# Optimization experiments

Hardware: AMD Instinct MI355X
Metric: run time of the kernel (lower is better)

Reference implementation:

```python
import jax, jax.numpy as jnp
import numpy as np

N, E = 100000, 1600000
IN, H, OUT, K = 512, 128, 128, 10
BN_EPS = 1e-5


def setup_inputs() -> dict:
    key = jax.random.key(0)
    ks = jax.random.split(key, 8)
    x = jax.random.normal(ks[0], (N, IN), dtype=jnp.float32)
    edge_index = jax.random.randint(ks[1], (2, E), 0, N, dtype=jnp.int64)
    W_enc = jax.random.normal(ks[2], (H, IN), dtype=jnp.float32) / np.sqrt(IN)
    b_enc = jnp.zeros((H,), dtype=jnp.float32)
    gammas = jax.random.normal(ks[3], (K + 1,), dtype=jnp.float32) * 0.3
    bn_gamma = jnp.ones((H,), dtype=jnp.float32)
    bn_beta = jnp.zeros((H,), dtype=jnp.float32)
    W_up = jax.random.normal(ks[4], (OUT, H), dtype=jnp.float32) / np.sqrt(H)
    b_up = jnp.zeros((OUT,), dtype=jnp.float32)
    prelu_alpha = jnp.array(0.25, dtype=jnp.float32)
    return dict(x=x, W_enc=W_enc, b_enc=b_enc, gammas=gammas,
                bn_gamma=bn_gamma, bn_beta=bn_beta, W_up=W_up, b_up=b_up,
                prelu_alpha=prelu_alpha, edge_index=edge_index, high_pass=1)


def reference(x, W_enc, b_enc, gammas, bn_gamma, bn_beta, W_up, b_up,
              prelu_alpha, edge_index, high_pass):
    n = x.shape[0]
    src, dst = edge_index[0], edge_index[1]

    # encoder (dropout p=0 -> identity)
    h = x @ W_enc.T + b_enc  # [N, H]

    # GCN-style symmetric normalization with self loops
    deg = jax.ops.segment_sum(jnp.ones_like(src, dtype=h.dtype), dst,
                              num_segments=n) + 1.0  # [N]
    w = jax.lax.rsqrt(deg[src] * deg[dst])  # [E]

    def adj(v):  # v: [N, H] -> A_hat @ v  (includes 1/deg self-loop term)
        msg = jax.ops.segment_sum(w[:, None] * v[src], dst, num_segments=n)
        return msg + v / deg[:, None]

    if high_pass:
        op = lambda v: v - adj(v)   # L_hat = I - A_hat
    else:
        op = adj

    # K-order polynomial filter: sum_k gamma_k * Op^k(h)
    def step(carry, g):
        hk, acc = carry
        hk = op(hk)
        return (hk, acc + g * hk), None

    (_, acc), _ = jax.lax.scan(step, (h, gammas[0] * h), gammas[1:])

    # BatchNorm1d over nodes (training-mode batch statistics)
    mu = jnp.mean(acc, axis=0)
    var = jnp.mean(jnp.square(acc - mu), axis=0)
    z = (acc - mu) * jax.lax.rsqrt(var + BN_EPS) * bn_gamma + bn_beta

    y = z @ W_up.T + b_up
    return jnp.where(y > 0, y, prelu_alpha * y)
```

## Files before the change

### kernel.cpp

```cpp
#include <hip/hip_runtime.h>
#include <hip/hip_fp16.h>

#define H_DIM 128
#define IN_DIM 512

typedef _Float16 half4v __attribute__((ext_vector_type(4)));
typedef _Float16 half8v __attribute__((ext_vector_type(8)));
typedef float f32x4 __attribute__((ext_vector_type(4)));

static inline size_t align256(size_t x) { return (x + 255) & ~(size_t)255; }


__global__ void count_deg_kernel(const int* __restrict__ dst, int* __restrict__ cnt, int e) {
    int i = blockIdx.x * blockDim.x + threadIdx.x;
    if (i < e) atomicAdd(&cnt[dst[i]], 1);
}

__global__ void deg_fin_kernel(const int* __restrict__ cnt, float* __restrict__ deg,
                               float* __restrict__ inv_deg, int n) {
    int i = blockIdx.x * blockDim.x + threadIdx.x;
    if (i < n) {
        float d = (float)cnt[i] + 1.0f;
        deg[i] = d;
        inv_deg[i] = 1.0f / d;
    }
}

__global__ void scan_a_kernel(const int* __restrict__ cnt, int* __restrict__ partial, int n) {
    __shared__ int sm[256];
    int i = blockIdx.x * 256 + threadIdx.x;
    sm[threadIdx.x] = (i < n) ? cnt[i] : 0;
    __syncthreads();
    for (int off = 128; off > 0; off >>= 1) {
        if (threadIdx.x < off) sm[threadIdx.x] += sm[threadIdx.x + off];
        __syncthreads();
    }
    if (threadIdx.x == 0) partial[blockIdx.x] = sm[0];
}

__global__ void scan_b_kernel(int* __restrict__ partial, int nb) {
    __shared__ int sm[512];
    int t = threadIdx.x;
    int v = (t < nb) ? partial[t] : 0;
    sm[t] = v;
    __syncthreads();
    for (int off = 1; off < 512; off <<= 1) {
        int u = (t >= off) ? sm[t - off] : 0;
        __syncthreads();
        sm[t] += u;
        __syncthreads();
    }
    if (t < nb) partial[t] = sm[t] - v;
}

__global__ void scan_c_kernel(const int* __restrict__ cnt, const int* __restrict__ partial,
                              int* __restrict__ row_start, int n) {
    __shared__ int sm[256];
    int i = blockIdx.x * 256 + threadIdx.x;
    int v = (i < n) ? cnt[i] : 0;
    sm[threadIdx.x] = v;
    __syncthreads();
    for (int off = 1; off < 256; off <<= 1) {
        int u = (threadIdx.x >= off) ? sm[threadIdx.x - off] : 0;
        __syncthreads();
        sm[threadIdx.x] += u;
        __syncthreads();
    }
    if (i < n) row_start[i + 1] = partial[blockIdx.x] + sm[threadIdx.x];
    if (i == 0) row_start[0] = 0;
}

__global__ void fill_csr_kernel(const int* __restrict__ src, const int* __restrict__ dst,
                                const float* __restrict__ deg, const int* __restrict__ row_start,
                                int* __restrict__ fill, int2* __restrict__ csr2, int e) {
    int i = blockIdx.x * blockDim.x + threadIdx.x;
    if (i < e) {
        int s = src[i], d = dst[i];
        int pos = row_start[d] + atomicAdd(&fill[d], 1);
        float w = 1.0f / sqrtf(deg[s] * deg[d]);
        csr2[pos] = make_int2(s, __float_as_int(w));
    }
}

__global__ __launch_bounds__(256) void encoder_mfma_kernel(
    const float* __restrict__ x, const float* __restrict__ W,
    const float* __restrict__ bias, const float* __restrict__ gammas,
    __half* __restrict__ h, __half* __restrict__ acc, int n) {
    __shared__ _Float16 As[64][64];
    __shared__ _Float16 Bs[128][64];
    const int tid = threadIdx.x;
    const int lane = tid & 63;
    const int wid = tid >> 6;
    const int wm = wid >> 1, wn = wid & 1;
    const int row0 = blockIdx.x * 64;
    const int lr = lane & 15;
    const int lk = (lane >> 4) * 8;
    f32x4 cacc[2][4];
#pragma unroll
    for (int a = 0; a < 2; ++a)
#pragma unroll
        for (int b = 0; b < 4; ++b) cacc[a][b] = (f32x4){0.f, 0.f, 0.f, 0.f};

    float4 xr[4], wr[8];
#pragma unroll
    for (int q = 0; q < 4; ++q) {
        int slot = tid * 4 + q;
        int r = slot >> 4, kq = (slot & 15) * 4;
        xr[q] = make_float4(0.f, 0.f, 0.f, 0.f);
        if (row0 + r < n) xr[q] = *(const float4*)&x[(size_t)(row0 + r) * IN_DIM + kq];
    }
#pragma unroll
    for (int q = 0; q < 8; ++q) {
        int slot = tid * 8 + q;
        int c = slot >> 4, kq = (slot & 15) * 4;
        wr[q] = *(const float4*)&W[(size_t)c * IN_DIM + kq];
    }

    for (int k0 = 0; k0 < IN_DIM; k0 += 64) {
#pragma unroll
        for (int q = 0; q < 4; ++q) {
            int slot = tid * 4 + q;
            int r = slot >> 4, kq = (slot & 15) * 4;
            int idx = kq ^ ((r & 7) << 3);
            half4v hv = {(_Float16)xr[q].x, (_Float16)xr[q].y, (_Float16)xr[q].z, (_Float16)xr[q].w};
            *(half4v*)&As[r][idx] = hv;
        }
#pragma unroll
        for (int q = 0; q < 8; ++q) {
            int slot = tid * 8 + q;
            int c = slot >> 4, kq = (slot & 15) * 4;
            int idx = kq ^ ((c & 7) << 3);
            half4v hv = {(_Float16)wr[q].x, (_Float16)wr[q].y, (_Float16)wr[q].z, (_Float16)wr[q].w};
            *(half4v*)&Bs[c][idx] = hv;
        }
        __syncthreads();
        if (k0 + 64 < IN_DIM) {
            int kn = k0 + 64;
#pragma unroll
            for (int q = 0; q < 4; ++q) {
                int slot = tid * 4 + q;
                int r = slot >> 4, kq = (slot & 15) * 4;
                xr[q] = make_float4(0.f, 0.f, 0.f, 0.f);
                if (row0 + r < n) xr[q] = *(const float4*)&x[(size_t)(row0 + r) * IN_DIM + kn + kq];
            }
#pragma unroll
            for (int q = 0; q < 8; ++q) {
                int slot = tid * 8 + q;
                int c = slot >> 4, kq = (slot & 15) * 4;
                wr[q] = *(const float4*)&W[(size_t)c * IN_DIM + kn + kq];
            }
        }
#pragma unroll
        for (int kk = 0; kk < 64; kk += 32) {
            half8v af[2], bf[4];
#pragma unroll
            for (int fm = 0; fm < 2; ++fm) {
                int r = wm * 32 + fm * 16 + lr;
                int kx = (kk + lk) ^ ((r & 7) << 3);
                af[fm] = *(const half8v*)&As[r][kx];
            }
#pragma unroll
            for (int fn = 0; fn < 4; ++fn) {
                int c = wn * 64 + fn * 16 + lr;
                int kx = (kk + lk) ^ ((c & 7) << 3);
                bf[fn] = *(const half8v*)&Bs[c][kx];
            }
#pragma unroll
            for (int fm = 0; fm < 2; ++fm)
#pragma unroll
                for (int fn = 0; fn < 4; ++fn)
                    cacc[fm][fn] = __builtin_amdgcn_mfma_f32_16x16x32_f16(
                        af[fm], bf[fn], cacc[fm][fn], 0, 0, 0);
        }
        __syncthreads();
    }
    const float g0 = gammas[0];
    const int orow = (lane >> 4) * 4;
#pragma unroll
    for (int fm = 0; fm < 2; ++fm) {
#pragma unroll
        for (int r = 0; r < 4; ++r) {
            int row = row0 + wm * 32 + fm * 16 + orow + r;
            if (row < n) {
#pragma unroll
                for (int fn = 0; fn < 4; ++fn) {
                    int col = wn * 64 + fn * 16 + lr;
                    float v = cacc[fm][fn][r] + bias[col];
                    h[(size_t)row * H_DIM + col] = __float2half(v);
                    acc[(size_t)row * H_DIM + col] = __float2half(g0 * v);
                }
            }
        }
    }
}

__global__ __launch_bounds__(256) void prop_kernel(
    const int* __restrict__ row_start, const int2* __restrict__ csr2,
    const float* __restrict__ inv_deg,
    const __half* __restrict__ hin, __half* __restrict__ hout,
    __half* __restrict__ acc, const float* __restrict__ gammas, int k,
    const int* __restrict__ hpp, int n) {
    const int w = threadIdx.x >> 6;
    const int l = threadIdx.x & 63;
    const int g = l >> 4;
    const int sub = l & 15;
    const int i = blockIdx.x * 4 + w;
    if (i >= n) return;
    const int beg = row_start[i], end = row_start[i + 1];
    const half8v* __restrict__ hin8 = (const half8v*)hin;
    float msg[8];
#pragma unroll
    for (int j = 0; j < 8; ++j) msg[j] = 0.f;
    int e = beg;
    for (; e + 8 <= end; e += 8) {
        int2 p0 = csr2[e + g];
        int2 p1 = csr2[e + 4 + g];
        half8v v0 = hin8[(size_t)p0.x * 16 + sub];
        half8v v1 = hin8[(size_t)p1.x * 16 + sub];
        float w0 = __int_as_float(p0.y), w1 = __int_as_float(p1.y);
#pragma unroll
        for (int j = 0; j < 8; ++j) {
            msg[j] = fmaf(w0, (float)v0[j], msg[j]);
            msg[j] = fmaf(w1, (float)v1[j], msg[j]);
        }
    }
    for (; e < end; e += 4) {
        int idx = e + g;
        int cidx = idx < end ? idx : end - 1;
        int2 p = csr2[cidx];
        float wgt = idx < end ? __int_as_float(p.y) : 0.f;
        half8v v = hin8[(size_t)p.x * 16 + sub];
#pragma unroll
        for (int j = 0; j < 8; ++j) msg[j] = fmaf(wgt, (float)v[j], msg[j]);
    }
#pragma unroll
    for (int j = 0; j < 8; ++j) {
        float m = msg[j];
        m += __shfl_xor(m, 16);
        m += __shfl_xor(m, 32);
        msg[j] = m;
    }
    const float idg = inv_deg[i];
    const half8v s8 = hin8[(size_t)i * 16 + sub];
    const int hp = *hpp;
    float hnew[8];
#pragma unroll
    for (int j = 0; j < 8; ++j) {
        float sf = (float)s8[j];
        float a = fmaf(sf, idg, msg[j]);
        hnew[j] = hp ? (sf - a) : a;
    }
    half8v* hout8 = (half8v*)hout;
    half8v* acc8 = (half8v*)acc;
    if (g == 0) {
        half8v h8;
#pragma unroll
        for (int j = 0; j < 8; ++j) h8[j] = (_Float16)hnew[j];
        hout8[(size_t)i * 16 + sub] = h8;
    } else if (g == 1) {
        const float gm = gammas[k];
        half8v av = acc8[(size_t)i * 16 + sub];
        half8v r;
#pragma unroll
        for (int j = 0; j < 8; ++j) r[j] = (_Float16)fmaf(gm, hnew[j], (float)av[j]);
        acc8[(size_t)i * 16 + sub] = r;
    }
}


__global__ __launch_bounds__(128) void bn_partial_kernel(const __half* __restrict__ acc,
                                                         float* __restrict__ sums, int n, int rpb) {
    int f = threadIdx.x;
    int r0 = blockIdx.x * rpb;
    int r1 = min(r0 + rpb, n);
    float s = 0.f, sq = 0.f;
    for (int r = r0; r < r1; ++r) {
        float v = __half2float(acc[(size_t)r * H_DIM + f]);
        s += v;
        sq = fmaf(v, v, sq);
    }
    atomicAdd(&sums[f], s);
    atomicAdd(&sums[H_DIM + f], sq);
}

__global__ __launch_bounds__(128) void bn_prep_kernel(
    const float* __restrict__ sums, const float* __restrict__ bn_gamma,
    const float* __restrict__ bn_beta, const float* __restrict__ W_up,
    const float* __restrict__ b_up, __half* __restrict__ W2h, float* __restrict__ cvec, int n) {
    __shared__ float ss[128], sh[128];
    int t = threadIdx.x;
    float nf = (float)n;
    float mu = sums[t] / nf;
    float var = sums[H_DIM + t] / nf - mu * mu;
    float sc = bn_gamma[t] / sqrtf(var + 1e-5f);
    float shv = bn_beta[t] - mu * sc;
    ss[t] = sc;
    sh[t] = shv;
    __syncthreads();
    float c = b_up[t];
    for (int hh = 0; hh < H_DIM; ++hh) {
        float wv = W_up[(size_t)t * H_DIM + hh];
        W2h[(size_t)t * H_DIM + hh] = __float2half(wv * ss[hh]);
        c = fmaf(wv, sh[hh], c);
    }
    cvec[t] = c;
}

__global__ __launch_bounds__(256) void final_mfma_kernel(
    const __half* __restrict__ accp, const __half* __restrict__ W2,
    const float* __restrict__ cvec, const float* __restrict__ alpha_p,
    float* __restrict__ out, int n) {
    __shared__ _Float16 As[64][128];
    __shared__ _Float16 Bs[128][128];
    const int tid = threadIdx.x;
    const int lane = tid & 63;
    const int wid = tid >> 6;
    const int wm = wid >> 1, wn = wid & 1;
    const int row0 = blockIdx.x * 64;
    const int lr = lane & 15;
    const int lk = (lane >> 4) * 8;
    f32x4 cacc[2][4];
#pragma unroll
    for (int a = 0; a < 2; ++a)
#pragma unroll
        for (int b = 0; b < 4; ++b) cacc[a][b] = (f32x4){0.f, 0.f, 0.f, 0.f};

#pragma unroll
    for (int q = 0; q < 4; ++q) {
        int slot = tid * 4 + q;
        int r = slot >> 4;
        int kq = (slot & 15) * 8;
        half8v av = {(_Float16)0, (_Float16)0, (_Float16)0, (_Float16)0,
                     (_Float16)0, (_Float16)0, (_Float16)0, (_Float16)0};
        if (row0 + r < n) av = *(const half8v*)&accp[(size_t)(row0 + r) * H_DIM + kq];
        int idx = kq ^ ((r & 7) << 3);
        *(half8v*)&As[r][idx] = av;
    }
#pragma unroll
    for (int q = 0; q < 8; ++q) {
        int slot = tid * 8 + q;
        int c = slot >> 4;
        int kq = (slot & 15) * 8;
        half8v wv = *(const half8v*)&W2[(size_t)c * H_DIM + kq];
        int idx = kq ^ ((c & 7) << 3);
        *(half8v*)&Bs[c][idx] = wv;
    }
    __syncthreads();
#pragma unroll
    for (int kk = 0; kk < 128; kk += 32) {
        half8v af[2], bf[4];
#pragma unroll
        for (int fm = 0; fm < 2; ++fm) {
            int r = wm * 32 + fm * 16 + lr;
            int kx = (kk + lk) ^ ((r & 7) << 3);
            af[fm] = *(const half8v*)&As[r][kx];
        }
#pragma unroll
        for (int fn = 0; fn < 4; ++fn) {
            int c = wn * 64 + fn * 16 + lr;
            int kx = (kk + lk) ^ ((c & 7) << 3);
            bf[fn] = *(const half8v*)&Bs[c][kx];
        }
#pragma unroll
        for (int fm = 0; fm < 2; ++fm)
#pragma unroll
            for (int fn = 0; fn < 4; ++fn)
                cacc[fm][fn] = __builtin_amdgcn_mfma_f32_16x16x32_f16(
                    af[fm], bf[fn], cacc[fm][fn], 0, 0, 0);
    }
    const float al = *alpha_p;
    const int orow = (lane >> 4) * 4;
#pragma unroll
    for (int fm = 0; fm < 2; ++fm) {
#pragma unroll
        for (int r = 0; r < 4; ++r) {
            int row = row0 + wm * 32 + fm * 16 + orow + r;
            if (row < n) {
#pragma unroll
                for (int fn = 0; fn < 4; ++fn) {
                    int col = wn * 64 + fn * 16 + lr;
                    float v = cacc[fm][fn][r] + cvec[col];
                    out[(size_t)row * H_DIM + col] = v > 0.f ? v : al * v;
                }
            }
        }
    }
}


extern "C" void kernel_launch(void* const* d_in, const int* in_sizes, int n_in,
                              void* d_out, int out_size, void* d_ws, size_t ws_size,
                              hipStream_t stream) {
    const float* x          = (const float*)d_in[0];
    const float* W_enc      = (const float*)d_in[1];
    const float* b_enc      = (const float*)d_in[2];
    const float* gammas     = (const float*)d_in[3];
    const float* bn_gamma   = (const float*)d_in[4];
    const float* bn_beta    = (const float*)d_in[5];
    const float* W_up       = (const float*)d_in[6];
    const float* b_up       = (const float*)d_in[7];
    const float* prelu_al   = (const float*)d_in[8];
    const int*   edge_index = (const int*)d_in[9];
    const int*   high_pass  = (const int*)d_in[10];

    const int H   = in_sizes[2];
    const int INF = in_sizes[1] / H;
    const int n   = in_sizes[0] / INF;
    const int e   = in_sizes[9] / 2;
    const int K   = in_sizes[3] - 1;

    const int* src = edge_index;
    const int* dst = edge_index + e;

    char* p = (char*)d_ws;
    auto alloc = [&](size_t bytes) -> char* { char* r = p; p += align256(bytes); return r; };
    int*    cnt       = (int*)alloc((size_t)n * 4);
    int*    fill      = (int*)alloc((size_t)n * 4);
    int*    row_start = (int*)alloc(((size_t)n + 1) * 4);
    int*    partial   = (int*)alloc(4096);
    float*  deg       = (float*)alloc((size_t)n * 4);
    float*  inv_deg   = (float*)alloc((size_t)n * 4);
    int2*   csr2      = (int2*)alloc(((size_t)e + 8) * 8);
    __half* hkA       = (__half*)alloc((size_t)n * H * 2);
    __half* hkB       = (__half*)alloc((size_t)n * H * 2);
    __half* acc       = (__half*)alloc((size_t)n * H * 2);
    float*  sums      = (float*)alloc(256 * 4);
    __half* W2h       = (__half*)alloc((size_t)H * H * 2);
    float*  cvec      = (float*)alloc((size_t)H * 4);

    hipMemsetAsync(cnt, 0, (size_t)n * 4, stream);
    hipMemsetAsync(fill, 0, (size_t)n * 4, stream);
    hipMemsetAsync(sums, 0, 256 * 4, stream);

    const int gb_e = (e + 255) / 256;
    const int gb_n = (n + 255) / 256;

    count_deg_kernel<<<gb_e, 256, 0, stream>>>(dst, cnt, e);
    deg_fin_kernel<<<gb_n, 256, 0, stream>>>(cnt, deg, inv_deg, n);
    scan_a_kernel<<<gb_n, 256, 0, stream>>>(cnt, partial, n);
    scan_b_kernel<<<1, 512, 0, stream>>>(partial, gb_n);
    scan_c_kernel<<<gb_n, 256, 0, stream>>>(cnt, partial, row_start, n);
    fill_csr_kernel<<<gb_e, 256, 0, stream>>>(src, dst, deg, row_start, fill, csr2, e);

    const int gb_m = (n + 63) / 64;
    encoder_mfma_kernel<<<gb_m, 256, 0, stream>>>(x, W_enc, b_enc, gammas, hkA, acc, n);

    __half* cur = hkA;
    __half* nxt = hkB;
    for (int k = 1; k <= K; ++k) {
        prop_kernel<<<(n + 3) / 4, 256, 0, stream>>>(row_start, csr2, inv_deg,
                                                     cur, nxt, acc, gammas, k, high_pass, n);
        __half* t = cur; cur = nxt; nxt = t;
    }

    const int nb_bn = 512;
    const int rpb = (n + nb_bn - 1) / nb_bn;
    bn_partial_kernel<<<nb_bn, 128, 0, stream>>>(acc, sums, n, rpb);
    bn_prep_kernel<<<1, 128, 0, stream>>>(sums, bn_gamma, bn_beta, W_up, b_up, W2h, cvec, n);
    final_mfma_kernel<<<gb_m, 256, 0, stream>>>(acc, W2h, cvec, prelu_al, (float*)d_out, n);
}
```

Measured before the change: 1.300 ms.

## Stage encoder tiles via direct global-to-LDS loads and unroll propagation gather

The encoder GEMM stops staging x and W through registers with a software prefetch. It now uses global_load_lds to copy swizzled fp32 x tiles and a pre-converted fp16 copy of W straight into shared memory, and converts A to fp16 when reading fragments. A small kernel that converts W to half is added, and the propagation kernel gains a 16-edge unrolled gather loop to keep more loads in flight. The trade-off is the loss of the register double-buffering overlap, a doubled LDS footprint for A, and an extra kernel launch.

```diff
diff --git a/kernel.cpp b/kernel.cpp
--- a/kernel.cpp
+++ b/kernel.cpp
@@ -9,6 +9,12 @@
 typedef float f32x4 __attribute__((ext_vector_type(4)));
 
 static inline size_t align256(size_t x) { return (x + 255) & ~(size_t)255; }
+
+__device__ inline void gload_lds16(const void* g, void* l) {
+    __builtin_amdgcn_global_load_lds(
+        (const __attribute__((address_space(1))) unsigned int*)g,
+        (__attribute__((address_space(3))) unsigned int*)l, 16, 0, 0);
+}
 
 
 __global__ void count_deg_kernel(const int* __restrict__ dst, int* __restrict__ cnt, int e) {
@@ -82,88 +88,72 @@
     }
 }
 
+__global__ void w_to_half_kernel(const float* __restrict__ W, __half* __restrict__ Wh, int total4) {
+    int i = blockIdx.x * blockDim.x + threadIdx.x;
+    if (i < total4) {
+        float4 v = *(const float4*)&W[i * 4];
+        half4v h = {(_Float16)v.x, (_Float16)v.y, (_Float16)v.z, (_Float16)v.w};
+        *(half4v*)&((_Float16*)Wh)[i * 4] = h;
+    }
+}
+
 __global__ __launch_bounds__(256) void encoder_mfma_kernel(
-    const float* __restrict__ x, const float* __restrict__ W,
+    const float* __restrict__ x, const __half* __restrict__ Wh,
     const float* __restrict__ bias, const float* __restrict__ gammas,
     __half* __restrict__ h, __half* __restrict__ acc, int n) {
-    __shared__ _Float16 As[64][64];
-    __shared__ _Float16 Bs[128][64];
+    __shared__ float As[64 * 64];
+    __shared__ _Float16 Bs[128 * 64];
     const int tid = threadIdx.x;
     const int lane = tid & 63;
     const int wid = tid >> 6;
     const int wm = wid >> 1, wn = wid & 1;
     const int row0 = blockIdx.x * 64;
     const int lr = lane & 15;
-    const int lk = (lane >> 4) * 8;
+    const int lk = lane >> 4;
     f32x4 cacc[2][4];
 #pragma unroll
     for (int a = 0; a < 2; ++a)
 #pragma unroll
         for (int b = 0; b < 4; ++b) cacc[a][b] = (f32x4){0.f, 0.f, 0.f, 0.f};
 
-    float4 xr[4], wr[8];
-#pragma unroll
-    for (int q = 0; q < 4; ++q) {
-        int slot = tid * 4 + q;
-        int r = slot >> 4, kq = (slot & 15) * 4;
-        xr[q] = make_float4(0.f, 0.f, 0.f, 0.f);
-        if (row0 + r < n) xr[q] = *(const float4*)&x[(size_t)(row0 + r) * IN_DIM + kq];
-    }
-#pragma unroll
-    for (int q = 0; q < 8; ++q) {
-        int slot = tid * 8 + q;
-        int c = slot >> 4, kq = (slot & 15) * 4;
-        wr[q] = *(const float4*)&W[(size_t)c * IN_DIM + kq];
-    }
-
     for (int k0 = 0; k0 < IN_DIM; k0 += 64) {
 #pragma unroll
         for (int q = 0; q < 4; ++q) {
-            int slot = tid * 4 + q;
-            int r = slot >> 4, kq = (slot & 15) * 4;
-            int idx = kq ^ ((r & 7) << 3);
-            half4v hv = {(_Float16)xr[q].x, (_Float16)xr[q].y, (_Float16)xr[q].z, (_Float16)xr[q].w};
-            *(half4v*)&As[r][idx] = hv;
-        }
-#pragma unroll
-        for (int q = 0; q < 8; ++q) {
-            int slot = tid * 8 + q;
-            int c = slot >> 4, kq = (slot & 15) * 4;
-            int idx = kq ^ ((c & 7) << 3);
-            half4v hv = {(_Float16)wr[q].x, (_Float16)wr[q].y, (_Float16)wr[q].z, (_Float16)wr[q].w};
-            *(half4v*)&Bs[c][idx] = hv;
-        }
-        __syncthreads();
-        if (k0 + 64 < IN_DIM) {
-            int kn = k0 + 64;
-#pragma unroll
-            for (int q = 0; q < 4; ++q) {
-                int slot = tid * 4 + q;
-                int r = slot >> 4, kq = (slot & 15) * 4;
-                xr[q] = make_float4(0.f, 0.f, 0.f, 0.f);
-                if (row0 + r < n) xr[q] = *(const float4*)&x[(size_t)(row0 + r) * IN_DIM + kn + kq];
-            }
-#pragma unroll
-            for (int q = 0; q < 8; ++q) {
-                int slot = tid * 8 + q;
-                int c = slot >> 4, kq = (slot & 15) * 4;
-                wr[q] = *(const float4*)&W[(size_t)c * IN_DIM + kn + kq];
-            }
-        }
+            int s = wid * 256 + q * 64 + lane;
+            int r = s >> 4, grp = s & 15;
+            int srow = (row0 + r < n) ? (row0 + r) : 0;
+            int col = k0 + ((grp ^ (r & 7)) << 2);
+            gload_lds16(&x[(size_t)srow * IN_DIM + col], &As[s * 4]);
+        }
+#pragma unroll
+        for (int q = 0; q < 4; ++q) {
+            int s = wid * 256 + q * 64 + lane;
+            int c = s >> 3, grp = s & 7;
+            int col = k0 + ((grp ^ (c & 7)) << 3);
+            gload_lds16(&((const _Float16*)Wh)[(size_t)c * IN_DIM + col], &Bs[s * 8]);
+        }
+        __syncthreads();
 #pragma unroll
         for (int kk = 0; kk < 64; kk += 32) {
             half8v af[2], bf[4];
 #pragma unroll
             for (int fm = 0; fm < 2; ++fm) {
                 int r = wm * 32 + fm * 16 + lr;
-                int kx = (kk + lk) ^ ((r & 7) << 3);
-                af[fm] = *(const half8v*)&As[r][kx];
+                int g0 = (kk >> 2) + (lk << 1);
+                int p0 = g0 ^ (r & 7), p1 = (g0 + 1) ^ (r & 7);
+                float4 a0 = *(const float4*)&As[r * 64 + p0 * 4];
+                float4 a1 = *(const float4*)&As[r * 64 + p1 * 4];
+                half8v v;
+                v[0] = (_Float16)a0.x; v[1] = (_Float16)a0.y; v[2] = (_Float16)a0.z; v[3] = (_Float16)a0.w;
+                v[4] = (_Float16)a1.x; v[5] = (_Float16)a1.y; v[6] = (_Float16)a1.z; v[7] = (_Float16)a1.w;
+                af[fm] = v;
             }
 #pragma unroll
             for (int fn = 0; fn < 4; ++fn) {
                 int c = wn * 64 + fn * 16 + lr;
-                int kx = (kk + lk) ^ ((c & 7) << 3);
-                bf[fn] = *(const half8v*)&Bs[c][kx];
+                int gl = (kk >> 3) + lk;
+                int pb = gl ^ (c & 7);
+                bf[fn] = *(const half8v*)&Bs[c * 64 + pb * 8];
             }
 #pragma unroll
             for (int fm = 0; fm < 2; ++fm)
@@ -174,7 +164,7 @@
         }
         __syncthreads();
     }
-    const float g0 = gammas[0];
+    const float g0v = gammas[0];
     const int orow = (lane >> 4) * 4;
 #pragma unroll
     for (int fm = 0; fm < 2; ++fm) {
@@ -187,7 +177,7 @@
                     int col = wn * 64 + fn * 16 + lr;
                     float v = cacc[fm][fn][r] + bias[col];
                     h[(size_t)row * H_DIM + col] = __float2half(v);
-                    acc[(size_t)row * H_DIM + col] = __float2half(g0 * v);
+                    acc[(size_t)row * H_DIM + col] = __float2half(g0v * v);
                 }
             }
         }
@@ -212,6 +202,25 @@
 #pragma unroll
     for (int j = 0; j < 8; ++j) msg[j] = 0.f;
     int e = beg;
+    for (; e + 16 <= end; e += 16) {
+        int2 p0 = csr2[e + g];
+        int2 p1 = csr2[e + 4 + g];
+        int2 p2 = csr2[e + 8 + g];
+        int2 p3 = csr2[e + 12 + g];
+        half8v v0 = hin8[(size_t)p0.x * 16 + sub];
+        half8v v1 = hin8[(size_t)p1.x * 16 + sub];
+        half8v v2 = hin8[(size_t)p2.x * 16 + sub];
+        half8v v3 = hin8[(size_t)p3.x * 16 + sub];
+        float w0 = __int_as_float(p0.y), w1 = __int_as_float(p1.y);
+        float w2 = __int_as_float(p2.y), w3 = __int_as_float(p3.y);
+#pragma unroll
+        for (int j = 0; j < 8; ++j) {
+            msg[j] = fmaf(w0, (float)v0[j], msg[j]);
+            msg[j] = fmaf(w1, (float)v1[j], msg[j]);
+            msg[j] = fmaf(w2, (float)v2[j], msg[j]);
+            msg[j] = fmaf(w3, (float)v3[j], msg[j]);
+        }
+    }
     for (; e + 8 <= end; e += 8) {
         int2 p0 = csr2[e + g];
         int2 p1 = csr2[e + 4 + g];
@@ -421,6 +430,7 @@
     float*  deg       = (float*)alloc((size_t)n * 4);
     float*  inv_deg   = (float*)alloc((size_t)n * 4);
     int2*   csr2      = (int2*)alloc(((size_t)e + 8) * 8);
+    __half* Wh        = (__half*)alloc((size_t)H * INF * 2);
     __half* hkA       = (__half*)alloc((size_t)n * H * 2);
     __half* hkB       = (__half*)alloc((size_t)n * H * 2);
     __half* acc       = (__half*)alloc((size_t)n * H * 2);
@@ -442,8 +452,11 @@
     scan_c_kernel<<<gb_n, 256, 0, stream>>>(cnt, partial, row_start, n);
     fill_csr_kernel<<<gb_e, 256, 0, stream>>>(src, dst, deg, row_start, fill, csr2, e);
 
+    const int wtotal4 = H * INF / 4;
+    w_to_half_kernel<<<(wtotal4 + 255) / 256, 256, 0, stream>>>(W_enc, Wh, wtotal4);
+
     const int gb_m = (n + 63) / 64;
-    encoder_mfma_kernel<<<gb_m, 256, 0, stream>>>(x, W_enc, b_enc, gammas, hkA, acc, n);
+    encoder_mfma_kernel<<<gb_m, 256, 0, stream>>>(x, Wh, b_enc, gammas, hkA, acc, n);
 
     __half* cur = hkA;
     __half* nxt = hkB;
```

Result: faster. 1.265 ms (-2.7%).
